# Kernel optimization log

Hardware: AMD Instinct MI355X
Metric: run time of the kernel (lower is better)

The kernel has to match this reference:

```python
import jax, jax.numpy as jnp
import numpy as np

B, T, D, H, HD = 2, 2048, 1024, 16, 64
NEG_INF = jnp.float32(-1e30)


def setup_inputs() -> dict:
    key = jax.random.key(0)
    ks = jax.random.split(key, 6)
    scale = 0.02
    return {
        "x": jax.random.normal(ks[0], (B, T, D), dtype=jnp.float32),
        "Wq": jax.random.normal(ks[1], (H, D, HD), dtype=jnp.float32) * scale,
        "Wk": jax.random.normal(ks[2], (H, D, HD), dtype=jnp.float32) * scale,
        "Wv": jax.random.normal(ks[3], (H, D, HD), dtype=jnp.float32) * scale,
        "Wp": jax.random.normal(ks[4], (D, H * HD), dtype=jnp.float32) * scale,
        "bp": jnp.zeros((D,), dtype=jnp.float32),
    }


def reference(x, Wq, Wk, Wv, Wp, bp):
    # Per-head QKV projections (stacked over heads): [B,H,T,HD]
    q = jnp.einsum("btd,hde->bhte", x, Wq)
    k = jnp.einsum("btd,hde->bhte", x, Wk)
    v = jnp.einsum("btd,hde->bhte", x, Wv)
    # Scaled scores [B,H,T,T] with causal mask, stable softmax
    scores = jnp.einsum("bhte,bhse->bhts", q, k) * (HD ** -0.5)
    causal = jnp.tril(jnp.ones((T, T), dtype=bool))
    scores = jnp.where(causal, scores, NEG_INF)
    attn = jax.nn.softmax(scores, axis=-1)
    out = jnp.einsum("bhts,bhse->bhte", attn, v)
    # Concat heads: [B,T,H*HD], then output projection (torch Linear: y = x @ W.T + b)
    concat = out.transpose(0, 2, 1, 3).reshape(B, T, H * HD)
    return concat @ Wp.T + bp
```

## Files before the change

### kernel.cpp

```cpp
#include <hip/hip_runtime.h>
#include <hip/hip_bf16.h>

#define TSEQ 2048
#define DM   1024
#define NH   16
#define HDIM 64
#define NB   2
#define BT   (NB*TSEQ)
#define QSCALE 0.1803368801111204f

typedef __attribute__((ext_vector_type(8))) short bf16x8;
typedef __attribute__((ext_vector_type(4))) float f32x4;

union BF8 { bf16x8 v; ushort u[8]; };

static __device__ __forceinline__ ushort f2b(float x) {
    unsigned u = __float_as_uint(x);
    return (ushort)((u + 0x7fff + ((u >> 16) & 1)) >> 16);
}

static __device__ __forceinline__ unsigned cvtpk(float lo, float hi) {
    unsigned r;
    asm("v_cvt_pk_bf16_f32 %0, %1, %2" : "=v"(r) : "v"(lo), "v"(hi));
    return r;
}

static __device__ __forceinline__ float fmax3(float a, float b, float c) {
    return fmaxf(fmaxf(a, b), c);
}

static __device__ __forceinline__ void gload16(const void* g, void* l) {
    __builtin_amdgcn_global_load_lds((const __attribute__((address_space(1))) void*)g,
                                     (__attribute__((address_space(3))) void*)l, 16, 0, 0);
}

__global__ __launch_bounds__(256) void cvt_kernel(const float* __restrict__ src,
                                                  ushort* __restrict__ dst, int n8) {
    int i = blockIdx.x * 256 + threadIdx.x;
    if (i >= n8) return;
    const float4* s = reinterpret_cast<const float4*>(src);
    float4 a = s[2*i], b = s[2*i+1];
    union { ushort u[8]; int4 v; } r;
    r.u[0]=f2b(a.x); r.u[1]=f2b(a.y); r.u[2]=f2b(a.z); r.u[3]=f2b(a.w);
    r.u[4]=f2b(b.x); r.u[5]=f2b(b.y); r.u[6]=f2b(b.z); r.u[7]=f2b(b.w);
    reinterpret_cast<int4*>(dst)[i] = r.v;
}

__global__ __launch_bounds__(256) void wt_kernel(const float* __restrict__ Wq,
                                                 const float* __restrict__ Wk,
                                                 const float* __restrict__ Wv,
                                                 ushort* __restrict__ wtb) {
    __shared__ float tile[64][65];
    const int t = threadIdx.x;
    const int k0 = blockIdx.x * 64;
    const int mat = blockIdx.y >> 4, h = blockIdx.y & 15;
    const float* W = (mat == 0 ? Wq : (mat == 1 ? Wk : Wv)) + (size_t)h * DM * HDIM;
#pragma unroll
    for (int it = 0; it < 4; ++it) {
        int row = it*16 + (t>>4), c4 = (t&15)*4;
        float4 v = *reinterpret_cast<const float4*>(&W[(size_t)(k0+row)*HDIM + c4]);
        tile[row][c4+0]=v.x; tile[row][c4+1]=v.y; tile[row][c4+2]=v.z; tile[row][c4+3]=v.w;
    }
    __syncthreads();
    ushort* out = wtb + (size_t)(mat*NH + h) * (HDIM*DM);
#pragma unroll
    for (int it = 0; it < 4; ++it) {
        int n = it*16 + (t>>4), kc = (t&15)*4;
        union { ushort u[4]; uint2 v; } r;
#pragma unroll
        for (int j = 0; j < 4; ++j) r.u[j] = f2b(tile[kc+j][n]);
        *reinterpret_cast<uint2*>(&out[(size_t)n*DM + k0 + kc]) = r.v;
    }
}

template<int EPI>
__global__ __launch_bounds__(256) void gemm_bt(const ushort* __restrict__ A,
                                               const ushort* __restrict__ B,
                                               const float* __restrict__ bias,
                                               void* __restrict__ C) {
    __shared__ ushort As[128*64];
    __shared__ ushort Bs[128*64];
    const int tid = threadIdx.x;
    const int w = tid >> 6, l = tid & 63;
    const int lr = l & 15, lg = l >> 4;
    const int wr = (w >> 1) * 64, wc = (w & 1) * 64;
    const int cpx = (int)gridDim.x >> 3;
    const int wg = ((int)blockIdx.x & 7) * cpx + ((int)blockIdx.x >> 3);
    const int m0 = (wg & 31) * 128;
    const int n0 = (wg >> 5) * 128;
    const int srow = l >> 3;
    const int scol = (l & 7) * 8;

    f32x4 acc[4][4];
#pragma unroll
    for (int a = 0; a < 4; ++a)
#pragma unroll
        for (int b = 0; b < 4; ++b) acc[a][b] = {0.f, 0.f, 0.f, 0.f};

    for (int kc = 0; kc < DM/64; ++kc) {
        __syncthreads();
#pragma unroll
        for (int c = 0; c < 4; ++c) {
            int chunk = w*4 + c;
            int r = chunk*8 + srow;
            gload16(&A[(size_t)(m0+r)*DM + kc*64 + scol], &As[chunk*512]);
            gload16(&B[(size_t)(n0+r)*DM + kc*64 + scol], &Bs[chunk*512]);
        }
        __syncthreads();
#pragma unroll
        for (int kk = 0; kk < 2; ++kk) {
            bf16x8 af[4], bf[4];
#pragma unroll
            for (int mf = 0; mf < 4; ++mf)
                af[mf] = *reinterpret_cast<const bf16x8*>(&As[(wr + mf*16 + lr)*64 + kk*32 + lg*8]);
#pragma unroll
            for (int nf = 0; nf < 4; ++nf)
                bf[nf] = *reinterpret_cast<const bf16x8*>(&Bs[(wc + nf*16 + lr)*64 + kk*32 + lg*8]);
            __builtin_amdgcn_s_setprio(1);
#pragma unroll
            for (int mf = 0; mf < 4; ++mf)
#pragma unroll
                for (int nf = 0; nf < 4; ++nf)
                    acc[mf][nf] = __builtin_amdgcn_mfma_f32_16x16x32_bf16(
                        af[mf], bf[nf], acc[mf][nf], 0, 0, 0);
            __builtin_amdgcn_s_setprio(0);
        }
    }

    if (EPI == 0) {
        ushort* O = (ushort*)C;
#pragma unroll
        for (int mf = 0; mf < 4; ++mf) {
#pragma unroll
            for (int i = 0; i < 4; ++i) {
                int m = m0 + wr + mf*16 + lg*4 + i;
                int bq = m >> 11, t = m & (TSEQ - 1);
#pragma unroll
                for (int nf = 0; nf < 4; ++nf) {
                    int col = n0 + wc + nf*16 + lr;
                    int mat = col >> 10, hh = (col >> 6) & 15, e = col & 63;
                    float sc = (mat == 0) ? QSCALE : 1.0f;
                    O[((size_t)(mat*2*NH + bq*NH + hh))*(TSEQ*HDIM) + (size_t)t*HDIM + e] =
                        f2b(acc[mf][nf][i] * sc);
                }
            }
        }
    } else {
        float* O = (float*)C;
#pragma unroll
        for (int mf = 0; mf < 4; ++mf) {
#pragma unroll
            for (int i = 0; i < 4; ++i) {
                int m = m0 + wr + mf*16 + lg*4 + i;
#pragma unroll
                for (int nf = 0; nf < 4; ++nf) {
                    int col = n0 + wc + nf*16 + lr;
                    O[(size_t)m*DM + col] = acc[mf][nf][i] + bias[col];
                }
            }
        }
    }
}

__global__ __launch_bounds__(256) void attn_mfma(const ushort* __restrict__ qkvb,
                                                 ushort* __restrict__ concatb) {
    __shared__ ushort Ks[2][64*64];
    __shared__ ushort Vt[2][64*64];
    __shared__ ushort Ps[4][32*64];
    const int tid = threadIdx.x;
    const int w = tid >> 6, l = tid & 63;
    const int lr = l & 15, lg = l >> 4;
    const int g = blockIdx.x;
    const int bh = (g & 7) * 4 + ((g >> 3) & 3);
    const int p  = g >> 5;
    const int qtHI = 16 + p, qtLO = 15 - p;
    const int qH0 = qtHI * 64 + w * 16;
    const int qL0 = qtLO * 64 + w * 16;

    const ushort* Q = qkvb + (size_t)bh * (TSEQ*HDIM);
    const ushort* K = Q + (size_t)2*NH*TSEQ*HDIM;
    const ushort* V = K + (size_t)2*NH*TSEQ*HDIM;

    bf16x8 qfH[2], qfL[2];
#pragma unroll
    for (int kk = 0; kk < 2; ++kk) {
        qfH[kk] = *reinterpret_cast<const bf16x8*>(&Q[(size_t)(qH0 + lr)*HDIM + kk*32 + lg*8]);
        qfL[kk] = *reinterpret_cast<const bf16x8*>(&Q[(size_t)(qL0 + lr)*HDIM + kk*32 + lg*8]);
    }

    f32x4 accH[4], accL[4];
    float mH = -3e38f, lH = 0.f, mL = -3e38f, lL = 0.f;
#pragma unroll
    for (int nf = 0; nf < 4; ++nf) { accH[nf] = {0.f,0.f,0.f,0.f}; accL[nf] = {0.f,0.f,0.f,0.f}; }

    ushort* PsW = &Ps[w][0];
    const int krow = tid >> 3, kchunk = (tid & 7) ^ ((tid >> 3) & 7);

    {
#pragma unroll
        for (int it = 0; it < 2; ++it)
            gload16(&K[(size_t)(it*32 + krow)*HDIM + kchunk*8], &Ks[0][it*2048 + tid*8]);
        BF8 a, b;
        a.v = *reinterpret_cast<const bf16x8*>(&V[(size_t)l*HDIM + w*16]);
        b.v = *reinterpret_cast<const bf16x8*>(&V[(size_t)l*HDIM + w*16 + 8]);
#pragma unroll
        for (int j = 0; j < 8; ++j) {
            Vt[0][(w*16 + j)*64 + ((l>>3) ^ j)*8 + (l&7)] = a.u[j];
            Vt[0][(w*16 + 8 + j)*64 + ((l>>3) ^ j)*8 + (l&7)] = b.u[j];
        }
        __syncthreads();
    }

    int cur = 0;
    for (int jt = 0; jt <= qtHI; ++jt) {
        const int nxt = cur ^ 1;
        const int s0 = jt * 64;
        const bool pref = (jt < qtHI);
        const bool loAct = (jt <= qtLO);
        BF8 ga, gb;
        if (pref) {
            const int s0n = s0 + 64;
#pragma unroll
            for (int it = 0; it < 2; ++it)
                gload16(&K[(size_t)(s0n + it*32 + krow)*HDIM + kchunk*8], &Ks[nxt][it*2048 + tid*8]);
            ga.v = *reinterpret_cast<const bf16x8*>(&V[(size_t)(s0n + l)*HDIM + w*16]);
            gb.v = *reinterpret_cast<const bf16x8*>(&V[(size_t)(s0n + l)*HDIM + w*16 + 8]);
        }

        f32x4 sH[4], sL[4];
#pragma unroll
        for (int nf = 0; nf < 4; ++nf) { sH[nf] = {0.f,0.f,0.f,0.f}; sL[nf] = {0.f,0.f,0.f,0.f}; }
#pragma unroll
        for (int kk = 0; kk < 2; ++kk) {
            bf16x8 kf[4];
#pragma unroll
            for (int nf = 0; nf < 4; ++nf)
                kf[nf] = *reinterpret_cast<const bf16x8*>(
                    &Ks[cur][(nf*16 + lr)*64 + ((kk*4 + lg) ^ (lr&7))*8]);
            __builtin_amdgcn_s_setprio(1);
#pragma unroll
            for (int nf = 0; nf < 4; ++nf)
                sH[nf] = __builtin_amdgcn_mfma_f32_16x16x32_bf16(kf[nf], qfH[kk], sH[nf], 0, 0, 0);
            if (loAct) {
#pragma unroll
                for (int nf = 0; nf < 4; ++nf)
                    sL[nf] = __builtin_amdgcn_mfma_f32_16x16x32_bf16(kf[nf], qfL[kk], sL[nf], 0, 0, 0);
            }
            __builtin_amdgcn_s_setprio(0);
        }

        {
            if (jt == qtHI) {
                int qrow = qH0 + lr;
#pragma unroll
                for (int nf = 0; nf < 4; ++nf) {
                    int kbase = s0 + nf*16 + lg*4;
#pragma unroll
                    for (int i = 0; i < 4; ++i)
                        if (kbase + i > qrow) sH[nf][i] = -1e30f;
                }
            }
            float g0 = fmax3(sH[0][0], sH[0][1], sH[0][2]);
            float g1 = fmax3(sH[0][3], sH[1][0], sH[1][1]);
            float g2 = fmax3(sH[1][2], sH[1][3], sH[2][0]);
            float g3 = fmax3(sH[2][1], sH[2][2], sH[2][3]);
            float g4 = fmax3(sH[3][0], sH[3][1], sH[3][2]);
            float tm = fmaxf(fmax3(fmax3(g0, g1, g2), g3, g4), sH[3][3]);
            tm = fmaxf(tm, __shfl_xor(tm, 16, 64));
            tm = fmaxf(tm, __shfl_xor(tm, 32, 64));
            if (__any(tm > mH + 8.0f)) {
                float mnew = fmaxf(mH, tm);
                float corr = exp2f(mH - mnew);
                lH *= corr;
#pragma unroll
                for (int nf = 0; nf < 4; ++nf)
#pragma unroll
                    for (int i = 0; i < 4; ++i) accH[nf][i] *= corr;
                mH = mnew;
            }
            float ps = 0.f;
#pragma unroll
            for (int nf = 0; nf < 4; ++nf)
#pragma unroll
                for (int i = 0; i < 4; ++i) { sH[nf][i] = exp2f(sH[nf][i] - mH); ps += sH[nf][i]; }
            ps += __shfl_xor(ps, 16, 64);
            ps += __shfl_xor(ps, 32, 64);
            lH += ps;
#pragma unroll
            for (int nf = 0; nf < 4; ++nf) {
                uint2 pk;
                pk.x = cvtpk(sH[nf][0], sH[nf][1]);
                pk.y = cvtpk(sH[nf][2], sH[nf][3]);
                *reinterpret_cast<uint2*>(
                    &PsW[lr*64 + ((2*nf + (lg>>1)) ^ (lr&7))*8 + (lg&1)*4]) = pk;
            }
        }
        if (loAct) {
            if (jt == qtLO) {
                int qrow = qL0 + lr;
#pragma unroll
                for (int nf = 0; nf < 4; ++nf) {
                    int kbase = s0 + nf*16 + lg*4;
#pragma unroll
                    for (int i = 0; i < 4; ++i)
                        if (kbase + i > qrow) sL[nf][i] = -1e30f;
                }
            }
            float g0 = fmax3(sL[0][0], sL[0][1], sL[0][2]);
            float g1 = fmax3(sL[0][3], sL[1][0], sL[1][1]);
            float g2 = fmax3(sL[1][2], sL[1][3], sL[2][0]);
            float g3 = fmax3(sL[2][1], sL[2][2], sL[2][3]);
            float g4 = fmax3(sL[3][0], sL[3][1], sL[3][2]);
            float tm = fmaxf(fmax3(fmax3(g0, g1, g2), g3, g4), sL[3][3]);
            tm = fmaxf(tm, __shfl_xor(tm, 16, 64));
            tm = fmaxf(tm, __shfl_xor(tm, 32, 64));
            if (__any(tm > mL + 8.0f)) {
                float mnew = fmaxf(mL, tm);
                float corr = exp2f(mL - mnew);
                lL *= corr;
#pragma unroll
                for (int nf = 0; nf < 4; ++nf)
#pragma unroll
                    for (int i = 0; i < 4; ++i) accL[nf][i] *= corr;
                mL = mnew;
            }
            float ps = 0.f;
#pragma unroll
            for (int nf = 0; nf < 4; ++nf)
#pragma unroll
                for (int i = 0; i < 4; ++i) { sL[nf][i] = exp2f(sL[nf][i] - mL); ps += sL[nf][i]; }
            ps += __shfl_xor(ps, 16, 64);
            ps += __shfl_xor(ps, 32, 64);
            lL += ps;
#pragma unroll
            for (int nf = 0; nf < 4; ++nf) {
                uint2 pk;
                pk.x = cvtpk(sL[nf][0], sL[nf][1]);
                pk.y = cvtpk(sL[nf][2], sL[nf][3]);
                *reinterpret_cast<uint2*>(
                    &PsW[(16 + lr)*64 + ((2*nf + (lg>>1)) ^ (lr&7))*8 + (lg&1)*4]) = pk;
            }
        }

#pragma unroll
        for (int kk = 0; kk < 2; ++kk) {
            bf16x8 vf[4];
#pragma unroll
            for (int nf = 0; nf < 4; ++nf)
                vf[nf] = *reinterpret_cast<const bf16x8*>(
                    &Vt[cur][(nf*16 + lr)*64 + ((kk*4 + lg) ^ (lr&7))*8]);
            bf16x8 pfH = *reinterpret_cast<const bf16x8*>(
                &PsW[lr*64 + ((kk*4 + lg) ^ (lr&7))*8]);
            __builtin_amdgcn_s_setprio(1);
#pragma unroll
            for (int nf = 0; nf < 4; ++nf)
                accH[nf] = __builtin_amdgcn_mfma_f32_16x16x32_bf16(vf[nf], pfH, accH[nf], 0, 0, 0);
            __builtin_amdgcn_s_setprio(0);
            if (loAct) {
                bf16x8 pfL = *reinterpret_cast<const bf16x8*>(
                    &PsW[(16 + lr)*64 + ((kk*4 + lg) ^ (lr&7))*8]);
                __builtin_amdgcn_s_setprio(1);
#pragma unroll
                for (int nf = 0; nf < 4; ++nf)
                    accL[nf] = __builtin_amdgcn_mfma_f32_16x16x32_bf16(vf[nf], pfL, accL[nf], 0, 0, 0);
                __builtin_amdgcn_s_setprio(0);
            }
        }

        if (pref) {
#pragma unroll
            for (int j = 0; j < 8; ++j) {
                Vt[nxt][(w*16 + j)*64 + ((l>>3) ^ j)*8 + (l&7)] = ga.u[j];
                Vt[nxt][(w*16 + 8 + j)*64 + ((l>>3) ^ j)*8 + (l&7)] = gb.u[j];
            }
        }
        __syncthreads();
        cur = nxt;
    }

    const int b = bh >> 4, h = bh & 15;
    {
        float inv = 1.0f / lH;
        int t = qH0 + lr;
        ushort* o = concatb + ((size_t)(b*TSEQ + t))*DM + h*HDIM;
#pragma unroll
        for (int nf = 0; nf < 4; ++nf) {
            uint2 pk;
            pk.x = cvtpk(accH[nf][0]*inv, accH[nf][1]*inv);
            pk.y = cvtpk(accH[nf][2]*inv, accH[nf][3]*inv);
            *reinterpret_cast<uint2*>(&o[nf*16 + lg*4]) = pk;
        }
    }
    {
        float inv = 1.0f / lL;
        int t = qL0 + lr;
        ushort* o = concatb + ((size_t)(b*TSEQ + t))*DM + h*HDIM;
#pragma unroll
        for (int nf = 0; nf < 4; ++nf) {
            uint2 pk;
            pk.x = cvtpk(accL[nf][0]*inv, accL[nf][1]*inv);
            pk.y = cvtpk(accL[nf][2]*inv, accL[nf][3]*inv);
            *reinterpret_cast<uint2*>(&o[nf*16 + lg*4]) = pk;
        }
    }
}

extern "C" void kernel_launch(void* const* d_in, const int* in_sizes, int n_in,
                              void* d_out, int out_size, void* d_ws, size_t ws_size,
                              hipStream_t stream) {
    const float* x  = (const float*)d_in[0];
    const float* Wq = (const float*)d_in[1];
    const float* Wk = (const float*)d_in[2];
    const float* Wv = (const float*)d_in[3];
    const float* Wp = (const float*)d_in[4];
    const float* bp = (const float*)d_in[5];
    float* out = (float*)d_out;

    ushort* ws   = (ushort*)d_ws;
    ushort* xb   = ws;
    ushort* wtb  = xb  + (size_t)BT*DM;
    ushort* wpb  = wtb + (size_t)3*NH*HDIM*DM;
    ushort* qkvb = wpb + (size_t)DM*DM;
    ushort* cb   = qkvb + (size_t)3*2*NH*TSEQ*HDIM;

    cvt_kernel<<<dim3((BT*DM/8 + 255)/256), 256, 0, stream>>>(x, xb, BT*DM/8);
    wt_kernel<<<dim3(DM/64, 3*NH), 256, 0, stream>>>(Wq, Wk, Wv, wtb);
    cvt_kernel<<<dim3(DM*DM/8/256), 256, 0, stream>>>(Wp, wpb, DM*DM/8);
    gemm_bt<0><<<dim3(32*24), 256, 0, stream>>>(xb, wtb, nullptr, qkvb);
    attn_mfma<<<dim3(512), 256, 0, stream>>>(qkvb, cb);
    gemm_bt<1><<<dim3(32*8), 256, 0, stream>>>(cb, wpb, bp, out);
}
```

Measured before the change: 141.1 us.

## Store V transposed from QKV GEMM and load it directly into LDS

The QKV projection epilogue now writes V in a transposed [e][t] layout, so the attention kernel can bring V tiles into LDS with async global_load_lds, just as it does for K. This removes the per-tile register round trip and the 16 scalar LDS stores per thread that transposed V inside the loop. In exchange the GEMM epilogue does strided 2-byte stores for the V part, which coalesce poorly.

```diff
diff --git a/kernel.cpp b/kernel.cpp
--- a/kernel.cpp
+++ b/kernel.cpp
@@ -11,8 +11,6 @@
 
 typedef __attribute__((ext_vector_type(8))) short bf16x8;
 typedef __attribute__((ext_vector_type(4))) float f32x4;
-
-union BF8 { bf16x8 v; ushort u[8]; };
 
 static __device__ __forceinline__ ushort f2b(float x) {
     unsigned u = __float_as_uint(x);
@@ -140,8 +138,9 @@
                     int col = n0 + wc + nf*16 + lr;
                     int mat = col >> 10, hh = (col >> 6) & 15, e = col & 63;
                     float sc = (mat == 0) ? QSCALE : 1.0f;
-                    O[((size_t)(mat*2*NH + bq*NH + hh))*(TSEQ*HDIM) + (size_t)t*HDIM + e] =
-                        f2b(acc[mf][nf][i] * sc);
+                    size_t base = (size_t)(mat*2*NH + bq*NH + hh) * (TSEQ*HDIM);
+                    size_t off = (mat == 2) ? ((size_t)e*TSEQ + t) : ((size_t)t*HDIM + e);
+                    O[base + off] = f2b(acc[mf][nf][i] * sc);
                 }
             }
         }
@@ -177,9 +176,9 @@
     const int qH0 = qtHI * 64 + w * 16;
     const int qL0 = qtLO * 64 + w * 16;
 
-    const ushort* Q = qkvb + (size_t)bh * (TSEQ*HDIM);
-    const ushort* K = Q + (size_t)2*NH*TSEQ*HDIM;
-    const ushort* V = K + (size_t)2*NH*TSEQ*HDIM;
+    const ushort* Q  = qkvb + (size_t)bh * (TSEQ*HDIM);
+    const ushort* K  = Q + (size_t)2*NH*TSEQ*HDIM;
+    const ushort* VT = K + (size_t)2*NH*TSEQ*HDIM;
 
     bf16x8 qfH[2], qfL[2];
 #pragma unroll
@@ -196,20 +195,12 @@
     ushort* PsW = &Ps[w][0];
     const int krow = tid >> 3, kchunk = (tid & 7) ^ ((tid >> 3) & 7);
 
-    {
-#pragma unroll
-        for (int it = 0; it < 2; ++it)
-            gload16(&K[(size_t)(it*32 + krow)*HDIM + kchunk*8], &Ks[0][it*2048 + tid*8]);
-        BF8 a, b;
-        a.v = *reinterpret_cast<const bf16x8*>(&V[(size_t)l*HDIM + w*16]);
-        b.v = *reinterpret_cast<const bf16x8*>(&V[(size_t)l*HDIM + w*16 + 8]);
-#pragma unroll
-        for (int j = 0; j < 8; ++j) {
-            Vt[0][(w*16 + j)*64 + ((l>>3) ^ j)*8 + (l&7)] = a.u[j];
-            Vt[0][(w*16 + 8 + j)*64 + ((l>>3) ^ j)*8 + (l&7)] = b.u[j];
-        }
-        __syncthreads();
-    }
+#pragma unroll
+    for (int it = 0; it < 2; ++it) {
+        gload16(&K [(size_t)(it*32 + krow)*HDIM + kchunk*8], &Ks[0][it*2048 + tid*8]);
+        gload16(&VT[(size_t)(it*32 + krow)*TSEQ + kchunk*8], &Vt[0][it*2048 + tid*8]);
+    }
+    __syncthreads();
 
     int cur = 0;
     for (int jt = 0; jt <= qtHI; ++jt) {
@@ -217,14 +208,13 @@
         const int s0 = jt * 64;
         const bool pref = (jt < qtHI);
         const bool loAct = (jt <= qtLO);
-        BF8 ga, gb;
         if (pref) {
             const int s0n = s0 + 64;
 #pragma unroll
-            for (int it = 0; it < 2; ++it)
-                gload16(&K[(size_t)(s0n + it*32 + krow)*HDIM + kchunk*8], &Ks[nxt][it*2048 + tid*8]);
-            ga.v = *reinterpret_cast<const bf16x8*>(&V[(size_t)(s0n + l)*HDIM + w*16]);
-            gb.v = *reinterpret_cast<const bf16x8*>(&V[(size_t)(s0n + l)*HDIM + w*16 + 8]);
+            for (int it = 0; it < 2; ++it) {
+                gload16(&K [(size_t)(s0n + it*32 + krow)*HDIM + kchunk*8], &Ks[nxt][it*2048 + tid*8]);
+                gload16(&VT[(size_t)(it*32 + krow)*TSEQ + s0n + kchunk*8], &Vt[nxt][it*2048 + tid*8]);
+            }
         }
 
         f32x4 sH[4], sL[4];
@@ -367,13 +357,6 @@
             }
         }
 
-        if (pref) {
-#pragma unroll
-            for (int j = 0; j < 8; ++j) {
-                Vt[nxt][(w*16 + j)*64 + ((l>>3) ^ j)*8 + (l&7)] = ga.u[j];
-                Vt[nxt][(w*16 + 8 + j)*64 + ((l>>3) ^ j)*8 + (l&7)] = gb.u[j];
-            }
-        }
         __syncthreads();
         cur = nxt;
     }
```

Result: slower. 153.4 us (+8.7%).

## Fuse prep kernels into one launch and rebalance causal attention tile pairing

Applied to the files above, without the earlier changes.

Merges the three conversion/transpose kernels into a single prep_kernel launch that dispatches on block index, removing two kernel launches. Changes the attention grid from 512 blocks, each pairing a high and low query tile, to 704 blocks. Large-work high tiles now run alone, while mid-range tiles are paired with small low tiles, so per-block causal work is more even. The attention loop now has to handle the missing low tile (qtLO = -1), which adds branching inside the hidden loop.

```diff
diff --git a/kernel.cpp b/kernel.cpp
--- a/kernel.cpp
+++ b/kernel.cpp
@@ -34,26 +34,32 @@
                                      (__attribute__((address_space(3))) void*)l, 16, 0, 0);
 }
 
-__global__ __launch_bounds__(256) void cvt_kernel(const float* __restrict__ src,
-                                                  ushort* __restrict__ dst, int n8) {
-    int i = blockIdx.x * 256 + threadIdx.x;
-    if (i >= n8) return;
-    const float4* s = reinterpret_cast<const float4*>(src);
-    float4 a = s[2*i], b = s[2*i+1];
-    union { ushort u[8]; int4 v; } r;
-    r.u[0]=f2b(a.x); r.u[1]=f2b(a.y); r.u[2]=f2b(a.z); r.u[3]=f2b(a.w);
-    r.u[4]=f2b(b.x); r.u[5]=f2b(b.y); r.u[6]=f2b(b.z); r.u[7]=f2b(b.w);
-    reinterpret_cast<int4*>(dst)[i] = r.v;
-}
-
-__global__ __launch_bounds__(256) void wt_kernel(const float* __restrict__ Wq,
-                                                 const float* __restrict__ Wk,
-                                                 const float* __restrict__ Wv,
-                                                 ushort* __restrict__ wtb) {
+__global__ __launch_bounds__(256) void prep_kernel(const float* __restrict__ x,
+                                                   const float* __restrict__ Wq,
+                                                   const float* __restrict__ Wk,
+                                                   const float* __restrict__ Wv,
+                                                   const float* __restrict__ Wp,
+                                                   ushort* __restrict__ xb,
+                                                   ushort* __restrict__ wpb,
+                                                   ushort* __restrict__ wtb) {
     __shared__ float tile[64][65];
-    const int t = threadIdx.x;
-    const int k0 = blockIdx.x * 64;
-    const int mat = blockIdx.y >> 4, h = blockIdx.y & 15;
+    const int g = blockIdx.x, t = threadIdx.x;
+    if (g < 2560) {
+        const float* src = (g < 2048) ? x : Wp;
+        ushort* dst = (g < 2048) ? xb : wpb;
+        int i = ((g < 2048) ? g : (g - 2048)) * 256 + t;
+        const float4* s = reinterpret_cast<const float4*>(src);
+        float4 a = s[2*i], b = s[2*i+1];
+        union { ushort u[8]; int4 v; } r;
+        r.u[0]=f2b(a.x); r.u[1]=f2b(a.y); r.u[2]=f2b(a.z); r.u[3]=f2b(a.w);
+        r.u[4]=f2b(b.x); r.u[5]=f2b(b.y); r.u[6]=f2b(b.z); r.u[7]=f2b(b.w);
+        reinterpret_cast<int4*>(dst)[i] = r.v;
+        return;
+    }
+    const int gb = g - 2560;
+    const int k0 = (gb & 15) * 64;
+    const int math = gb >> 4;
+    const int mat = math >> 4, h = math & 15;
     const float* W = (mat == 0 ? Wq : (mat == 1 ? Wk : Wv)) + (size_t)h * DM * HDIM;
 #pragma unroll
     for (int it = 0; it < 4; ++it) {
@@ -171,9 +177,11 @@
     const int w = tid >> 6, l = tid & 63;
     const int lr = l & 15, lg = l >> 4;
     const int g = blockIdx.x;
-    const int bh = (g & 7) * 4 + ((g >> 3) & 3);
-    const int p  = g >> 5;
-    const int qtHI = 16 + p, qtLO = 15 - p;
+    const int sb = g >> 5;
+    const int bhid = g & 31;
+    const int bh = (bhid & 7) * 4 + (bhid >> 3);
+    const int qtHI = (sb == 21) ? 10 : 31 - sb;
+    const int qtLO = (sb >= 11 && sb <= 20) ? (sb - 11) : -1;
     const int qH0 = qtHI * 64 + w * 16;
     const int qL0 = qtLO * 64 + w * 16;
 
@@ -183,9 +191,12 @@
 
     bf16x8 qfH[2], qfL[2];
 #pragma unroll
-    for (int kk = 0; kk < 2; ++kk) {
+    for (int kk = 0; kk < 2; ++kk)
         qfH[kk] = *reinterpret_cast<const bf16x8*>(&Q[(size_t)(qH0 + lr)*HDIM + kk*32 + lg*8]);
-        qfL[kk] = *reinterpret_cast<const bf16x8*>(&Q[(size_t)(qL0 + lr)*HDIM + kk*32 + lg*8]);
+    if (qtLO >= 0) {
+#pragma unroll
+        for (int kk = 0; kk < 2; ++kk)
+            qfL[kk] = *reinterpret_cast<const bf16x8*>(&Q[(size_t)(qL0 + lr)*HDIM + kk*32 + lg*8]);
     }
 
     f32x4 accH[4], accL[4];
@@ -391,7 +402,7 @@
             *reinterpret_cast<uint2*>(&o[nf*16 + lg*4]) = pk;
         }
     }
-    {
+    if (qtLO >= 0) {
         float inv = 1.0f / lL;
         int t = qL0 + lr;
         ushort* o = concatb + ((size_t)(b*TSEQ + t))*DM + h*HDIM;
@@ -423,10 +434,8 @@
     ushort* qkvb = wpb + (size_t)DM*DM;
     ushort* cb   = qkvb + (size_t)3*2*NH*TSEQ*HDIM;
 
-    cvt_kernel<<<dim3((BT*DM/8 + 255)/256), 256, 0, stream>>>(x, xb, BT*DM/8);
-    wt_kernel<<<dim3(DM/64, 3*NH), 256, 0, stream>>>(Wq, Wk, Wv, wtb);
-    cvt_kernel<<<dim3(DM*DM/8/256), 256, 0, stream>>>(Wp, wpb, DM*DM/8);
+    prep_kernel<<<dim3(3328), 256, 0, stream>>>(x, Wq, Wk, Wv, Wp, xb, wpb, wtb);
     gemm_bt<0><<<dim3(32*24), 256, 0, stream>>>(xb, wtb, nullptr, qkvb);
-    attn_mfma<<<dim3(512), 256, 0, stream>>>(qkvb, cb);
+    attn_mfma<<<dim3(704), 256, 0, stream>>>(qkvb, cb);
     gemm_bt<1><<<dim3(32*8), 256, 0, stream>>>(cb, wpb, bp, out);
 }
```

After: 145.3 us. +3.0%, slower.
